# Optimization experiments

Measured on AMD Instinct MI355X. Metric: run time of the kernel, lower is better.

## Reference

```python
import jax, jax.numpy as jnp
import numpy as np

B, T, E = 32, 2048, 1024

def setup_inputs() -> dict:
    key = jax.random.key(0)
    k1, k2, k3 = jax.random.split(key, 3)
    enc = jax.random.normal(k1, (B, T, E), dtype=jnp.float32)
    ctx = jax.random.normal(k2, (B, E), dtype=jnp.float32)
    W = jax.random.normal(k3, (E, E), dtype=jnp.float32) * 0.05
    b = jnp.zeros((1, E), dtype=jnp.float32)
    return {"enc": enc, "ctx": ctx, "W": W, "b": b}

def reference(enc, ctx, W, b):
    # ht: (B, T, E) = tanh(enc @ W + b)
    ht = jnp.tanh(jnp.einsum('bte,ef->btf', enc, W) + b)
    # scores: (B, T) = batch dot of ctx against each timestep of ht
    scores = jnp.einsum('be,bte->bt', ctx, ht)
    at = jax.nn.softmax(scores, axis=-1)
    # weighted sum pooling over time -> (B, E)
    return jnp.einsum('bt,bte->be', at, ht)
```

## Files before the change

kernel.cpp:

```cpp
#include <hip/hip_runtime.h>
#include <hip/hip_bf16.h>
#include <math.h>

typedef unsigned short u16;
typedef unsigned int   u32;
typedef _Float16 f16x8 __attribute__((ext_vector_type(8)));
typedef float f32x4  __attribute__((ext_vector_type(4)));

#define Bb 32
#define Tt 2048
#define Ee 1024
#define Mm (Bb*Tt)

__device__ __forceinline__ float tanh_fast(float x) {
  float ax = fminf(fabsf(x), 15.0f);
  float e  = __expf(2.0f * ax);
  float t  = 1.0f - 2.0f / (e + 1.0f);
  return copysignf(t, x);
}

__device__ __forceinline__ u32 pack2h(float a, float b) {
  _Float16 ha = (_Float16)a, hb = (_Float16)b;
  return (u32)__builtin_bit_cast(u16, ha) | ((u32)__builtin_bit_cast(u16, hb) << 16);
}

__device__ __forceinline__ void glds16(const u16* g, u16* l) {
  __builtin_amdgcn_global_load_lds(
      (const __attribute__((address_space(1))) void*)g,
      (__attribute__((address_space(3))) void*)l, 16, 0, 0);
}

__global__ __launch_bounds__(256) void wt_convert(const float* __restrict__ W,
                                                  u16* __restrict__ Wt_hi,
                                                  u16* __restrict__ Wt_lo) {
  __shared__ float tile[32][33];
  int n0 = blockIdx.x * 32, k0 = blockIdx.y * 32;
  int tx = threadIdx.x, ty = threadIdx.y;
#pragma unroll
  for (int i = 0; i < 4; ++i)
    tile[ty + 8*i][tx] = W[(size_t)(k0 + ty + 8*i) * Ee + n0 + tx];
  __syncthreads();
#pragma unroll
  for (int i = 0; i < 4; ++i) {
    float v = tile[tx][ty + 8*i];
    _Float16 hi = (_Float16)v;
    float rem = v - (float)hi;
    _Float16 lo = (_Float16)rem;
    size_t idx = (size_t)(n0 + ty + 8*i) * Ee + k0 + tx;
    Wt_hi[idx] = __builtin_bit_cast(u16, hi);
    Wt_lo[idx] = __builtin_bit_cast(u16, lo);
  }
}

__global__ __launch_bounds__(256, 3) void gemm_tanh_score(
    const float* __restrict__ enc, const float* __restrict__ ctx,
    const float* __restrict__ bias,
    const u16* __restrict__ Wt_hi, const u16* __restrict__ Wt_lo,
    u16* __restrict__ ht, float* __restrict__ scores) {
  __shared__ __align__(16) u16 Ah[2*4096];
  __shared__ __align__(16) u16 BhS[2*4096];
  __shared__ __align__(16) u16 BlS[2*4096];

  int bx = blockIdx.x;
  int xcd = bx & 7, lb = bx >> 3;
  int nt = lb & 7, mtl = lb >> 3;
  int mt = xcd * 64 + mtl;
  int m0 = mt * 128, n0 = nt * 128;

  int tid = threadIdx.x;
  int w = tid >> 6, lane = tid & 63;
  int wm = (w & 1) * 64, wn = (w >> 1) * 64;
  int q = lane >> 4, c = lane & 15;
  int fch = (q ^ ((c >> 1) & 3)) * 8;

  f32x4 zero = {0.f, 0.f, 0.f, 0.f};
  f32x4 acc[4][4];
#pragma unroll
  for (int i = 0; i < 4; ++i)
#pragma unroll
    for (int j = 0; j < 4; ++j) acc[i][j] = zero;

  int ar = tid >> 1, ah = tid & 1;
  const float4* Abase = (const float4*)(enc + (size_t)(m0 + ar) * Ee + ah * 16);
  int awr = ar * 32;
  int asw = (ar >> 1) & 3;
  int ac0 = ((2*ah + 0) ^ asw) * 8;
  int ac1 = ((2*ah + 1) ^ asw) * 8;

  int cidx0 = w * 2, cidx1 = w * 2 + 1;
  int r0 = cidx0 * 16 + (lane >> 2);
  int r1 = cidx1 * 16 + (lane >> 2);
  int lg0 = ((lane & 3) ^ ((r0 >> 1) & 3)) * 8;
  int lg1 = ((lane & 3) ^ ((r1 >> 1) & 3)) * 8;
  const u16* Bh0 = Wt_hi + (size_t)(n0 + r0) * Ee + lg0;
  const u16* Bh1 = Wt_hi + (size_t)(n0 + r1) * Ee + lg1;
  const u16* Bl0 = Wt_lo + (size_t)(n0 + r0) * Ee + lg0;
  const u16* Bl1 = Wt_lo + (size_t)(n0 + r1) * Ee + lg1;
  int bws0 = cidx0 * 512, bws1 = cidx1 * 512;

  {
    float4 f0 = Abase[0], f1 = Abase[1], f2 = Abase[2], f3 = Abase[3];
    glds16(Bh0, &BhS[bws0]);
    glds16(Bh1, &BhS[bws1]);
    glds16(Bl0, &BlS[bws0]);
    glds16(Bl1, &BlS[bws1]);
    u32 p0 = pack2h(f0.x, f0.y), p1 = pack2h(f0.z, f0.w);
    u32 p2 = pack2h(f1.x, f1.y), p3 = pack2h(f1.z, f1.w);
    u32 p4 = pack2h(f2.x, f2.y), p5 = pack2h(f2.z, f2.w);
    u32 p6 = pack2h(f3.x, f3.y), p7 = pack2h(f3.z, f3.w);
    *(uint4*)&Ah[awr + ac0] = make_uint4(p0, p1, p2, p3);
    *(uint4*)&Ah[awr + ac1] = make_uint4(p4, p5, p6, p7);
    __syncthreads();
  }

#pragma unroll 2
  for (int kt = 0; kt < 32; ++kt) {
    int cur = (kt & 1) * 4096, nxt = 4096 - cur;
    float4 f0, f1, f2, f3;
    if (kt < 31) {
      const float4* ap = Abase + (size_t)(kt + 1) * 8;
      f0 = ap[0]; f1 = ap[1]; f2 = ap[2]; f3 = ap[3];
      size_t ko = (size_t)(kt + 1) * 32;
      glds16(Bh0 + ko, &BhS[nxt + bws0]);
      glds16(Bh1 + ko, &BhS[nxt + bws1]);
      glds16(Bl0 + ko, &BlS[nxt + bws0]);
      glds16(Bl1 + ko, &BlS[nxt + bws1]);
    }

    f16x8 aF[4];
#pragma unroll
    for (int i = 0; i < 4; ++i)
      aF[i] = *(const f16x8*)&Ah[cur + (wm + i*16 + c) * 32 + fch];

    __builtin_amdgcn_s_setprio(1);
#pragma unroll
    for (int j = 0; j < 4; ++j) {
      f16x8 bH = *(const f16x8*)&BhS[cur + (wn + j*16 + c) * 32 + fch];
      f16x8 bL = *(const f16x8*)&BlS[cur + (wn + j*16 + c) * 32 + fch];
#pragma unroll
      for (int i = 0; i < 4; ++i) {
        acc[i][j] = __builtin_amdgcn_mfma_f32_16x16x32_f16(aF[i], bH, acc[i][j], 0, 0, 0);
        acc[i][j] = __builtin_amdgcn_mfma_f32_16x16x32_f16(aF[i], bL, acc[i][j], 0, 0, 0);
      }
    }
    __builtin_amdgcn_s_setprio(0);

    if (kt < 31) {
      u32 p0 = pack2h(f0.x, f0.y), p1 = pack2h(f0.z, f0.w);
      u32 p2 = pack2h(f1.x, f1.y), p3 = pack2h(f1.z, f1.w);
      u32 p4 = pack2h(f2.x, f2.y), p5 = pack2h(f2.z, f2.w);
      u32 p6 = pack2h(f3.x, f3.y), p7 = pack2h(f3.z, f3.w);
      *(uint4*)&Ah[nxt + awr + ac0] = make_uint4(p0, p1, p2, p3);
      *(uint4*)&Ah[nxt + awr + ac1] = make_uint4(p4, p5, p6, p7);
    }
    __syncthreads();
  }

  int bidx = m0 >> 11;
  float ctxv[4], biasv[4];
#pragma unroll
  for (int j = 0; j < 4; ++j) {
    int col = n0 + wn + j * 16 + c;
    ctxv[j]  = ctx[bidx * Ee + col];
    biasv[j] = bias[col];
  }
#pragma unroll
  for (int i = 0; i < 4; ++i) {
#pragma unroll
    for (int r = 0; r < 4; ++r) {
      int rowG = m0 + wm + i * 16 + q * 4 + r;
      u16* hrow = ht + (size_t)rowG * Ee + n0 + wn + c;
      float s = 0.f;
#pragma unroll
      for (int j = 0; j < 4; ++j) {
        float h = tanh_fast(acc[i][j][r] + biasv[j]);
        __hip_bfloat16 hb = __float2bfloat16(h);
        hrow[j * 16] = *(u16*)&hb;
        s += h * ctxv[j];
      }
      s += __shfl_xor(s, 1); s += __shfl_xor(s, 2);
      s += __shfl_xor(s, 4); s += __shfl_xor(s, 8);
      if (c == 0) atomicAdd(&scores[rowG], s);
    }
  }
}

__global__ __launch_bounds__(256) void softmax_t(const float* __restrict__ scores,
                                                 float* __restrict__ at) {
  __shared__ float red[256];
  int b = blockIdx.x, tid = threadIdx.x;
  float v[8];
  float mx = -3.0e38f;
#pragma unroll
  for (int i = 0; i < 8; ++i) {
    v[i] = scores[b * Tt + i * 256 + tid];
    mx = fmaxf(mx, v[i]);
  }
  red[tid] = mx; __syncthreads();
  for (int s = 128; s > 0; s >>= 1) {
    if (tid < s) red[tid] = fmaxf(red[tid], red[tid + s]);
    __syncthreads();
  }
  mx = red[0]; __syncthreads();
  float sum = 0.f;
#pragma unroll
  for (int i = 0; i < 8; ++i) { v[i] = __expf(v[i] - mx); sum += v[i]; }
  red[tid] = sum; __syncthreads();
  for (int s = 128; s > 0; s >>= 1) {
    if (tid < s) red[tid] += red[tid + s];
    __syncthreads();
  }
  float inv = 1.0f / red[0];
#pragma unroll
  for (int i = 0; i < 8; ++i) at[b * Tt + i * 256 + tid] = v[i] * inv;
}

__global__ __launch_bounds__(256) void weighted_sum(const u16* __restrict__ ht,
                                                    const float* __restrict__ at,
                                                    float* __restrict__ part) {
  __shared__ float ats[64];
  int bx = blockIdx.x;
  int b = bx >> 5, tc = bx & 31;
  int tid = threadIdx.x;
  if (tid < 64) ats[tid] = at[b * Tt + tc * 64 + tid];
  __syncthreads();
  int e0 = tid * 4;
  const u16* base = ht + (size_t)(b * Tt + tc * 64) * Ee + e0;
  float s0 = 0.f, s1 = 0.f, s2 = 0.f, s3 = 0.f;
#pragma unroll 4
  for (int t = 0; t < 64; ++t) {
    float a = ats[t];
    uint2 u = *(const uint2*)(base + (size_t)t * Ee);
    s0 += a * __uint_as_float(u.x << 16);
    s1 += a * __uint_as_float(u.x & 0xffff0000u);
    s2 += a * __uint_as_float(u.y << 16);
    s3 += a * __uint_as_float(u.y & 0xffff0000u);
  }
  float4 out4 = make_float4(s0, s1, s2, s3);
  *(float4*)(part + ((size_t)(b * 32 + tc) * Ee + e0)) = out4;
}

__global__ __launch_bounds__(256) void reduce_part(const float* __restrict__ part,
                                                   float* __restrict__ out) {
  int b = blockIdx.x, tid = threadIdx.x;
  float4 s = make_float4(0.f, 0.f, 0.f, 0.f);
#pragma unroll
  for (int tc = 0; tc < 32; ++tc) {
    float4 p = ((const float4*)(part + (size_t)(b * 32 + tc) * Ee))[tid];
    s.x += p.x; s.y += p.y; s.z += p.z; s.w += p.w;
  }
  ((float4*)(out + (size_t)b * Ee))[tid] = s;
}

extern "C" void kernel_launch(void* const* d_in, const int* in_sizes, int n_in,
                              void* d_out, int out_size, void* d_ws, size_t ws_size,
                              hipStream_t stream) {
  const float* enc  = (const float*)d_in[0];
  const float* ctx  = (const float*)d_in[1];
  const float* W    = (const float*)d_in[2];
  const float* bias = (const float*)d_in[3];
  float* out = (float*)d_out;

  char* ws = (char*)d_ws;
  u16* Wt_hi = (u16*)(ws);
  u16* Wt_lo = (u16*)(ws + (size_t)2 * 1024 * 1024);
  u16* ht    = (u16*)(ws + (size_t)4 * 1024 * 1024);
  float* scores = (float*)(ws + (size_t)4 * 1024 * 1024 + (size_t)Mm * Ee * 2);
  float* at     = scores + Mm;
  float* part   = (float*)ws;

  hipMemsetAsync(scores, 0, (size_t)Mm * sizeof(float), stream);

  wt_convert<<<dim3(32, 32), dim3(32, 8), 0, stream>>>(W, Wt_hi, Wt_lo);
  gemm_tanh_score<<<dim3(4096), dim3(256), 0, stream>>>(enc, ctx, bias, Wt_hi, Wt_lo, ht, scores);
  softmax_t<<<dim3(32), dim3(256), 0, stream>>>(scores, at);
  weighted_sum<<<dim3(1024), dim3(256), 0, stream>>>(ht, at, part);
  reduce_part<<<dim3(32), dim3(256), 0, stream>>>(part, out);
}
```

Measured before the change: 690.0 us.

## Enlarge GEMM M-tile to 256 rows per block to reuse W tiles

Doubles the M dimension of each GEMM block from 128 to 256 rows. Each wave now computes 128x64 outputs with 8x4 accumulators, the A staging buffer doubles, and the grid halves to 2048 blocks. The aim is to halve the repeated loads of the hi/lo W tiles and raise the MFMA-to-load ratio. In exchange it raises register pressure (launch bounds drop to 2 waves per SIMD) and lowers occupancy.

```diff
diff --git a/kernel.cpp b/kernel.cpp
--- a/kernel.cpp
+++ b/kernel.cpp
@@ -52,40 +52,37 @@
   }
 }
 
-__global__ __launch_bounds__(256, 3) void gemm_tanh_score(
+__global__ __launch_bounds__(256, 2) void gemm_tanh_score(
     const float* __restrict__ enc, const float* __restrict__ ctx,
     const float* __restrict__ bias,
     const u16* __restrict__ Wt_hi, const u16* __restrict__ Wt_lo,
     u16* __restrict__ ht, float* __restrict__ scores) {
-  __shared__ __align__(16) u16 Ah[2*4096];
+  __shared__ __align__(16) u16 Ah [2*8192];
   __shared__ __align__(16) u16 BhS[2*4096];
   __shared__ __align__(16) u16 BlS[2*4096];
 
   int bx = blockIdx.x;
   int xcd = bx & 7, lb = bx >> 3;
   int nt = lb & 7, mtl = lb >> 3;
-  int mt = xcd * 64 + mtl;
-  int m0 = mt * 128, n0 = nt * 128;
+  int mt = xcd * 32 + mtl;
+  int m0 = mt * 256, n0 = nt * 128;
 
   int tid = threadIdx.x;
   int w = tid >> 6, lane = tid & 63;
-  int wm = (w & 1) * 64, wn = (w >> 1) * 64;
+  int wm = (w & 1) * 128, wn = (w >> 1) * 64;
   int q = lane >> 4, c = lane & 15;
   int fch = (q ^ ((c >> 1) & 3)) * 8;
 
   f32x4 zero = {0.f, 0.f, 0.f, 0.f};
-  f32x4 acc[4][4];
-#pragma unroll
-  for (int i = 0; i < 4; ++i)
+  f32x4 acc[8][4];
+#pragma unroll
+  for (int i = 0; i < 8; ++i)
 #pragma unroll
     for (int j = 0; j < 4; ++j) acc[i][j] = zero;
 
-  int ar = tid >> 1, ah = tid & 1;
-  const float4* Abase = (const float4*)(enc + (size_t)(m0 + ar) * Ee + ah * 16);
-  int awr = ar * 32;
-  int asw = (ar >> 1) & 3;
-  int ac0 = ((2*ah + 0) ^ asw) * 8;
-  int ac1 = ((2*ah + 1) ^ asw) * 8;
+  int arow = tid >> 3, ac8 = tid & 7;
+  const float4* Abase = (const float4*)enc + ((size_t)(m0 + arow) * Ee >> 2) + ac8;
+  int awbase = arow * 32 + (((ac8 >> 1) ^ ((arow >> 1) & 3)) << 3) + (ac8 & 1) * 4;
 
   int cidx0 = w * 2, cidx1 = w * 2 + 1;
   int r0 = cidx0 * 16 + (lane >> 2);
@@ -99,46 +96,48 @@
   int bws0 = cidx0 * 512, bws1 = cidx1 * 512;
 
   {
-    float4 f0 = Abase[0], f1 = Abase[1], f2 = Abase[2], f3 = Abase[3];
     glds16(Bh0, &BhS[bws0]);
     glds16(Bh1, &BhS[bws1]);
     glds16(Bl0, &BlS[bws0]);
     glds16(Bl1, &BlS[bws1]);
-    u32 p0 = pack2h(f0.x, f0.y), p1 = pack2h(f0.z, f0.w);
-    u32 p2 = pack2h(f1.x, f1.y), p3 = pack2h(f1.z, f1.w);
-    u32 p4 = pack2h(f2.x, f2.y), p5 = pack2h(f2.z, f2.w);
-    u32 p6 = pack2h(f3.x, f3.y), p7 = pack2h(f3.z, f3.w);
-    *(uint4*)&Ah[awr + ac0] = make_uint4(p0, p1, p2, p3);
-    *(uint4*)&Ah[awr + ac1] = make_uint4(p4, p5, p6, p7);
+    float4 av[8];
+#pragma unroll
+    for (int p = 0; p < 8; ++p) av[p] = Abase[(size_t)(32 * p) * (Ee / 4)];
+#pragma unroll
+    for (int p = 0; p < 8; ++p)
+      *(uint2*)&Ah[awbase + 1024 * p] =
+          make_uint2(pack2h(av[p].x, av[p].y), pack2h(av[p].z, av[p].w));
     __syncthreads();
   }
 
 #pragma unroll 2
   for (int kt = 0; kt < 32; ++kt) {
-    int cur = (kt & 1) * 4096, nxt = 4096 - cur;
-    float4 f0, f1, f2, f3;
+    int curA = (kt & 1) * 8192, nxtA = 8192 - curA;
+    int curB = (kt & 1) * 4096, nxtB = 4096 - curB;
+    float4 av[8];
     if (kt < 31) {
-      const float4* ap = Abase + (size_t)(kt + 1) * 8;
-      f0 = ap[0]; f1 = ap[1]; f2 = ap[2]; f3 = ap[3];
+#pragma unroll
+      for (int p = 0; p < 8; ++p)
+        av[p] = Abase[(size_t)(32 * p) * (Ee / 4) + (kt + 1) * 8];
       size_t ko = (size_t)(kt + 1) * 32;
-      glds16(Bh0 + ko, &BhS[nxt + bws0]);
-      glds16(Bh1 + ko, &BhS[nxt + bws1]);
-      glds16(Bl0 + ko, &BlS[nxt + bws0]);
-      glds16(Bl1 + ko, &BlS[nxt + bws1]);
-    }
-
-    f16x8 aF[4];
-#pragma unroll
-    for (int i = 0; i < 4; ++i)
-      aF[i] = *(const f16x8*)&Ah[cur + (wm + i*16 + c) * 32 + fch];
+      glds16(Bh0 + ko, &BhS[nxtB + bws0]);
+      glds16(Bh1 + ko, &BhS[nxtB + bws1]);
+      glds16(Bl0 + ko, &BlS[nxtB + bws0]);
+      glds16(Bl1 + ko, &BlS[nxtB + bws1]);
+    }
+
+    f16x8 aF[8];
+#pragma unroll
+    for (int i = 0; i < 8; ++i)
+      aF[i] = *(const f16x8*)&Ah[curA + (wm + i * 16 + c) * 32 + fch];
 
     __builtin_amdgcn_s_setprio(1);
 #pragma unroll
     for (int j = 0; j < 4; ++j) {
-      f16x8 bH = *(const f16x8*)&BhS[cur + (wn + j*16 + c) * 32 + fch];
-      f16x8 bL = *(const f16x8*)&BlS[cur + (wn + j*16 + c) * 32 + fch];
-#pragma unroll
-      for (int i = 0; i < 4; ++i) {
+      f16x8 bH = *(const f16x8*)&BhS[curB + (wn + j * 16 + c) * 32 + fch];
+      f16x8 bL = *(const f16x8*)&BlS[curB + (wn + j * 16 + c) * 32 + fch];
+#pragma unroll
+      for (int i = 0; i < 8; ++i) {
         acc[i][j] = __builtin_amdgcn_mfma_f32_16x16x32_f16(aF[i], bH, acc[i][j], 0, 0, 0);
         acc[i][j] = __builtin_amdgcn_mfma_f32_16x16x32_f16(aF[i], bL, acc[i][j], 0, 0, 0);
       }
@@ -146,12 +145,10 @@
     __builtin_amdgcn_s_setprio(0);
 
     if (kt < 31) {
-      u32 p0 = pack2h(f0.x, f0.y), p1 = pack2h(f0.z, f0.w);
-      u32 p2 = pack2h(f1.x, f1.y), p3 = pack2h(f1.z, f1.w);
-      u32 p4 = pack2h(f2.x, f2.y), p5 = pack2h(f2.z, f2.w);
-      u32 p6 = pack2h(f3.x, f3.y), p7 = pack2h(f3.z, f3.w);
-      *(uint4*)&Ah[nxt + awr + ac0] = make_uint4(p0, p1, p2, p3);
-      *(uint4*)&Ah[nxt + awr + ac1] = make_uint4(p4, p5, p6, p7);
+#pragma unroll
+      for (int p = 0; p < 8; ++p)
+        *(uint2*)&Ah[nxtA + awbase + 1024 * p] =
+            make_uint2(pack2h(av[p].x, av[p].y), pack2h(av[p].z, av[p].w));
     }
     __syncthreads();
   }
@@ -165,7 +162,7 @@
     biasv[j] = bias[col];
   }
 #pragma unroll
-  for (int i = 0; i < 4; ++i) {
+  for (int i = 0; i < 8; ++i) {
 #pragma unroll
     for (int r = 0; r < 4; ++r) {
       int rowG = m0 + wm + i * 16 + q * 4 + r;
@@ -272,7 +269,7 @@
   hipMemsetAsync(scores, 0, (size_t)Mm * sizeof(float), stream);
 
   wt_convert<<<dim3(32, 32), dim3(32, 8), 0, stream>>>(W, Wt_hi, Wt_lo);
-  gemm_tanh_score<<<dim3(4096), dim3(256), 0, stream>>>(enc, ctx, bias, Wt_hi, Wt_lo, ht, scores);
+  gemm_tanh_score<<<dim3(2048), dim3(256), 0, stream>>>(enc, ctx, bias, Wt_hi, Wt_lo, ht, scores);
   softmax_t<<<dim3(32), dim3(256), 0, stream>>>(scores, at);
   weighted_sum<<<dim3(1024), dim3(256), 0, stream>>>(ht, at, part);
   reduce_part<<<dim3(32), dim3(256), 0, stream>>>(part, out);
```

Result: faster. 652.0 us (-5.5%).
